# Kernel tuning notes

Hardware: AMD Instinct MI355X
Metric: run time of the kernel (lower is better)

Reference implementation:

```python
import jax, jax.numpy as jnp
import numpy as np

ROPE_THETA = 10000.0

def rope(x):
    # RoPE over the FULL model_dim (applied pre head-split, as in the source),
    # interleaved even/odd pairs. x: [B, S, D]
    B, S, D = x.shape
    half = D // 2
    inv_freq = 1.0 / (ROPE_THETA ** (jnp.arange(half, dtype=jnp.float32) * 2.0 / D))
    ang = jnp.arange(S, dtype=jnp.float32)[:, None] * inv_freq[None, :]  # [S, half]
    cos, sin = jnp.cos(ang), jnp.sin(ang)
    x1, x2 = x[..., 0::2], x[..., 1::2]
    r1 = x1 * cos - x2 * sin
    r2 = x1 * sin + x2 * cos
    return jnp.stack([r1, r2], axis=-1).reshape(B, S, D)


def setup_inputs() -> dict:
    key = jax.random.key(0)
    ks = jax.random.split(key, 9)
    B, S, D = 4, 2048, 768
    w = 0.02
    return {
        "X":  jax.random.normal(ks[0], (B, S, D), dtype=jnp.float32),
        "Wq": jax.random.normal(ks[1], (D, D), dtype=jnp.float32) * w,
        "bq": jnp.zeros((D,), dtype=jnp.float32),
        "Wk": jax.random.normal(ks[2], (D, D), dtype=jnp.float32) * w,
        "bk": jnp.zeros((D,), dtype=jnp.float32),
        "Wv": jax.random.normal(ks[3], (D, D), dtype=jnp.float32) * w,
        "bv": jnp.zeros((D,), dtype=jnp.float32),
        "Wo": jax.random.normal(ks[4], (D, D), dtype=jnp.float32) * w,
        "bo": jnp.zeros((D,), dtype=jnp.float32),
    }


def reference(X, Wq, bq, Wk, bk, Wv, bv, Wo, bo):
    NUM_HEADS = 12
    B, S, D = X.shape
    hd = D // NUM_HEADS

    q = rope(X @ Wq + bq)   # RoPE applied pre-split on full model_dim
    k = rope(X @ Wk + bk)
    v = X @ Wv + bv

    # Contiguous per-head slices == reshape to [B, S, H, hd]
    qh = q.reshape(B, S, NUM_HEADS, hd)
    kh = k.reshape(B, S, NUM_HEADS, hd)
    vh = v.reshape(B, S, NUM_HEADS, hd)

    scores = jnp.einsum('bqhd,bkhd->bhqk', qh, kh) / jnp.sqrt(jnp.float32(hd))
    causal = jnp.tril(jnp.ones((S, S), dtype=bool))
    scores = jnp.where(causal[None, None, :, :], scores, -jnp.inf)
    weights = jax.nn.softmax(scores, axis=-1)
    out = jnp.einsum('bhqk,bkhd->bqhd', weights, vh).reshape(B, S, D)
    return out @ Wo + bo
```

## Files before the change

### kernel.cpp

```cpp
#include <hip/hip_runtime.h>
#include <math.h>

#define D_MODEL 768
#define NUM_HEADS 12
#define HEAD_DIM 64
#define SEQ 2048
#define BATCH 4
#define MROWS (BATCH * SEQ)
#define HALF_D (D_MODEL / 2)

typedef __bf16    bf16x8 __attribute__((ext_vector_type(8)));
typedef _Float16  f16x4  __attribute__((ext_vector_type(4)));
typedef float     f32x4  __attribute__((ext_vector_type(4)));

__device__ __forceinline__ void gload_lds16(const void* gp, void* lp) {
    __builtin_amdgcn_global_load_lds(
        (const __attribute__((address_space(1))) unsigned int*)gp,
        (__attribute__((address_space(3))) unsigned int*)lp, 16, 0, 0);
}

__global__ __launch_bounds__(256)
void prep(const float* __restrict__ X, __bf16* __restrict__ Xb,
          const float* __restrict__ W0, const float* __restrict__ W1,
          const float* __restrict__ W2, const float* __restrict__ W3,
          __bf16* __restrict__ T0, __bf16* __restrict__ T1,
          __bf16* __restrict__ T2, __bf16* __restrict__ T3)
{
    __shared__ float t[64][65];
    const int n   = blockIdx.x;
    const int tid = threadIdx.x;

    if (n < 3072) {
        size_t i = ((size_t)n * 256 + tid) * 8;
        float4 u = *(const float4*)(X + i);
        float4 v = *(const float4*)(X + i + 4);
        bf16x8 o;
        o[0]=(__bf16)u.x; o[1]=(__bf16)u.y; o[2]=(__bf16)u.z; o[3]=(__bf16)u.w;
        o[4]=(__bf16)v.x; o[5]=(__bf16)v.y; o[6]=(__bf16)v.z; o[7]=(__bf16)v.w;
        *(bf16x8*)(Xb + i) = o;
    } else {
        int m = n - 3072;
        int z = m / 144;
        int rem = m - z * 144;
        int by = rem / 12, bx = rem % 12;
        const float* W = z == 0 ? W0 : z == 1 ? W1 : z == 2 ? W2 : W3;
        __bf16*      T = z == 0 ? T0 : z == 1 ? T1 : z == 2 ? T2 : T3;

        const int r0 = by * 64, c0 = bx * 64;
        const int lx = tid & 63, g = tid >> 6;

        #pragma unroll
        for (int rr = 0; rr < 16; ++rr) {
            int r = g * 16 + rr;
            t[r][lx] = W[(size_t)(r0 + r) * D_MODEL + c0 + lx];
        }
        __syncthreads();

        const int nn = tid >> 2;
        const int kb = (tid & 3) * 16;
        bf16x8 o1, o2;
        #pragma unroll
        for (int mm = 0; mm < 8; ++mm) o1[mm] = (__bf16)t[kb + mm][nn];
        #pragma unroll
        for (int mm = 0; mm < 8; ++mm) o2[mm] = (__bf16)t[kb + 8 + mm][nn];
        __bf16* dst = T + (size_t)(c0 + nn) * D_MODEL + r0 + kb;
        *(bf16x8*)dst       = o1;
        *(bf16x8*)(dst + 8) = o2;
    }
}

__global__ __launch_bounds__(512, 6)
void qkv_gemm(const __bf16* __restrict__ Xb,
              const __bf16* __restrict__ Wqt, const __bf16* __restrict__ Wkt,
              const __bf16* __restrict__ Wvt,
              const float* __restrict__ bq, const float* __restrict__ bk,
              const float* __restrict__ bv,
              __bf16* __restrict__ Qb, __bf16* __restrict__ Kb,
              _Float16* __restrict__ Vtb)
{
    __shared__ bf16x8 Asf[3][8][64];
    __shared__ bf16x8 Bsf[3][8][64];

    const int tid  = threadIdx.x;
    const int wv   = tid >> 6;
    const int ln   = tid & 63;
    const int t15  = ln & 15;
    const int quad = ln >> 4;
    const int wr = wv >> 2, wc = wv & 3;

    const int lin = blockIdx.x;
    const int c   = lin >> 6;
    const int r   = lin & 63;
    const int which = c / 6;
    const int col0  = (c % 6) * 128;
    const int row0  = r * 128;

    const __bf16* Wt  = which == 0 ? Wqt : which == 1 ? Wkt : Wvt;
    const float* bias = which == 0 ? bq  : which == 1 ? bk  : bv;

    f32x4 acc[4][2];
    #pragma unroll
    for (int i = 0; i < 4; ++i)
        #pragma unroll
        for (int j = 0; j < 2; ++j) acc[i][j] = (f32x4){0.f,0.f,0.f,0.f};

    const __bf16* seg[2];
    bf16x8*       dstp[2];
    #pragma unroll
    for (int u = 0; u < 2; ++u) {
        const int id   = wv * 2 + u;
        const int isB  = id >> 3;
        const int slot = id & 7;
        const __bf16* base = isB
            ? Wt + (size_t)(col0 + 16 * slot + t15) * D_MODEL
            : Xb + (size_t)(row0 + 16 * slot + t15) * D_MODEL;
        seg[u]  = base + 8 * quad;
        dstp[u] = isB ? &Bsf[0][slot][0] : &Asf[0][slot][0];
    }

    auto stage = [&](int buf, int k0) {
        #pragma unroll
        for (int u = 0; u < 2; ++u)
            gload_lds16(seg[u] + k0, dstp[u] + buf * 512);
    };

    stage(0, 0);
    stage(1, 32);

    const int NT = D_MODEL / 32;
    int cur = 0, nx = 2;
    for (int t = 0; t < NT; ++t) {
        if (t < NT - 1) { asm volatile("s_waitcnt vmcnt(2)" ::: "memory"); }
        else            { asm volatile("s_waitcnt vmcnt(0)" ::: "memory"); }
        __builtin_amdgcn_s_barrier();
        if (t + 2 < NT) stage(nx, 32 * (t + 2));

        bf16x8 af[4], bfr[2];
        #pragma unroll
        for (int i = 0; i < 4; ++i) af[i]  = Asf[cur][4 * wr + i][ln];
        #pragma unroll
        for (int j = 0; j < 2; ++j) bfr[j] = Bsf[cur][2 * wc + j][ln];
        #pragma unroll
        for (int i = 0; i < 4; ++i)
            #pragma unroll
            for (int j = 0; j < 2; ++j)
                acc[i][j] = __builtin_amdgcn_mfma_f32_16x16x32_bf16(af[i], bfr[j], acc[i][j], 0, 0, 0);

        cur = (cur == 2) ? 0 : cur + 1;
        nx  = (nx  == 2) ? 0 : nx  + 1;
    }

    if (which < 2) {
        const float oscale = (which == 0) ? 0.125f : 1.0f;
        __bf16* dstq = which ? Kb : Qb;
        #pragma unroll
        for (int i = 0; i < 4; ++i) {
            const int rowb = row0 + 64 * wr + 16 * i + 4 * quad;
            const int s0   = rowb & (SEQ - 1);
            #pragma unroll
            for (int j = 0; j < 2; ++j) {
                const int col = col0 + 32 * wc + 16 * j + t15;
                const float bval = bias[col];
                const int ne = col & ~1;
                const float fr = __expf((float)ne * (-9.210340371976184f / 768.0f));
                const float cf = __cosf(fr), sf = __sinf(fr);
                const float sgn = (col & 1) ? 1.0f : -1.0f;
                float ang = (float)s0 * fr;
                float ca = __cosf(ang), sa = __sinf(ang);
                #pragma unroll
                for (int rr = 0; rr < 4; ++rr) {
                    const int rw = rowb + rr;
                    float val  = acc[i][j][rr] + bval;
                    float part = __shfl_xor(val, 1, 64);
                    dstq[(size_t)rw * D_MODEL + col] = (__bf16)((val * ca + part * sgn * sa) * oscale);
                    float cn = ca * cf - sa * sf;
                    sa = sa * cf + ca * sf;
                    ca = cn;
                }
            }
        }
    } else {
        #pragma unroll
        for (int i = 0; i < 4; ++i) {
            const int rowb = row0 + 64 * wr + 16 * i + 4 * quad;
            #pragma unroll
            for (int j = 0; j < 2; ++j) {
                const int col = col0 + 32 * wc + 16 * j + t15;
                const float bval = bias[col];
                const int h = col >> 6, d = col & 63;
                const int bidx = rowb >> 11, s = rowb & (SEQ - 1);
                f16x4 pk;
                #pragma unroll
                for (int rr = 0; rr < 4; ++rr) pk[rr] = (_Float16)(acc[i][j][rr] + bval);
                *(f16x4*)(Vtb + ((size_t)(bidx * NUM_HEADS + h) * 64 + d) * SEQ + s) = pk;
            }
        }
    }
}

__global__ __launch_bounds__(256)
void out_gemm(const __bf16* __restrict__ Ab, const __bf16* __restrict__ Wt,
              const float* __restrict__ bias, float* __restrict__ Cout)
{
    __shared__ bf16x8 Asf[3][4][64];
    __shared__ bf16x8 Bsf[3][8][64];

    const int tid  = threadIdx.x;
    const int wv   = tid >> 6;
    const int ln   = tid & 63;
    const int t15  = ln & 15;
    const int quad = ln >> 4;
    const int wr = wv >> 1, wc = wv & 1;

    const int lin  = blockIdx.x;
    const int col0 = (lin >> 7) * 128;
    const int row0 = (lin & 127) * 64;

    f32x4 acc[2][4];
    #pragma unroll
    for (int i = 0; i < 2; ++i)
        #pragma unroll
        for (int j = 0; j < 4; ++j) acc[i][j] = (f32x4){0.f,0.f,0.f,0.f};

    auto stage = [&](int buf, int k0) {
        #pragma unroll
        for (int u = 0; u < 3; ++u) {
            const int id = wv * 3 + u;
            if (id < 4) {
                const __bf16* src = Ab + (size_t)(row0 + 16 * id + t15) * D_MODEL
                                       + k0 + 8 * quad;
                gload_lds16(src, &Asf[buf][id][0]);
            } else {
                const int w = id - 4;
                const __bf16* src = Wt + (size_t)(col0 + 16 * w + t15) * D_MODEL
                                       + k0 + 8 * quad;
                gload_lds16(src, &Bsf[buf][w][0]);
            }
        }
    };

    stage(0, 0);
    stage(1, 32);
    stage(2, 64);

    const int NT = D_MODEL / 32;
    int cur = 0;
    for (int t = 0; t < NT; ++t) {
        if (t + 2 < NT)      { asm volatile("s_waitcnt vmcnt(6)" ::: "memory"); }
        else if (t + 1 < NT) { asm volatile("s_waitcnt vmcnt(3)" ::: "memory"); }
        else                 { asm volatile("s_waitcnt vmcnt(0)" ::: "memory"); }
        __builtin_amdgcn_s_barrier();

        bf16x8 af[2], bfr[4];
        #pragma unroll
        for (int i = 0; i < 2; ++i) af[i]  = Asf[cur][2 * wr + i][ln];
        #pragma unroll
        for (int j = 0; j < 4; ++j) bfr[j] = Bsf[cur][4 * wc + j][ln];
        #pragma unroll
        for (int i = 0; i < 2; ++i)
            #pragma unroll
            for (int j = 0; j < 4; ++j)
                acc[i][j] = __builtin_amdgcn_mfma_f32_16x16x32_bf16(af[i], bfr[j], acc[i][j], 0, 0, 0);

        asm volatile("s_waitcnt lgkmcnt(0)" ::: "memory");
        __builtin_amdgcn_s_barrier();
        if (t + 3 < NT) stage(cur, 32 * (t + 3));
        cur = (cur == 2) ? 0 : cur + 1;
    }

    #pragma unroll
    for (int i = 0; i < 2; ++i) {
        const int rowb = row0 + 32 * wr + 16 * i + 4 * quad;
        #pragma unroll
        for (int j = 0; j < 4; ++j) {
            const int col = col0 + 64 * wc + 16 * j + t15;
            const float bval = bias[col];
            #pragma unroll
            for (int rr = 0; rr < 4; ++rr)
                Cout[(size_t)(rowb + rr) * D_MODEL + col] = acc[i][j][rr] + bval;
        }
    }
}

__device__ __forceinline__ void attn_tile(
    const bf16x8 (*Kbuf)[64], const _Float16* Vbuf ,
    bf16x8 aq0, bf16x8 aq1,
    f32x4* o, float& lacc,
    int ln, int t15, int quad, int j0, int qglob, bool domask)
{
    f32x4 s[4];
    #pragma unroll
    for (int c = 0; c < 4; ++c) {
        s[c] = (f32x4){0.f, 0.f, 0.f, 0.f};
        s[c] = __builtin_amdgcn_mfma_f32_16x16x32_bf16(Kbuf[c][ln],     aq0, s[c], 0, 0, 0);
        s[c] = __builtin_amdgcn_mfma_f32_16x16x32_bf16(Kbuf[4 + c][ln], aq1, s[c], 0, 0, 0);
    }

    f16x4 pf[4];
    #pragma unroll
    for (int c = 0; c < 4; ++c)
        #pragma unroll
        for (int r = 0; r < 4; ++r) {
            float e = __expf(s[c][r]);
            if (domask && (j0 + 16 * c + 4 * quad + r > qglob)) e = 0.f;
            lacc += e;
            pf[c][r] = (_Float16)e;
        }

    #pragma unroll
    for (int c = 0; c < 4; ++c) {
        const int lv = 16 * (2 * (c & 1) + (quad >> 1)) + t15;
        const int jb = 4 * (quad & 1);
        #pragma unroll
        for (int cd = 0; cd < 4; ++cd) {
            f16x4 vf = *(const f16x4*)&Vbuf[(size_t)(4 * (c >> 1) + cd) * 512 + lv * 8 + jb];
            o[cd] = __builtin_amdgcn_mfma_f32_16x16x16f16(pf[c], vf, o[cd], 0, 0, 0);
        }
    }
}

__global__ __launch_bounds__(512)
void attn_flash(const __bf16* __restrict__ Q, const __bf16* __restrict__ K,
                const _Float16* __restrict__ Vt, __bf16* __restrict__ O)
{
    __shared__ bf16x8   Kf[2][8][64];
    __shared__ _Float16 Vh[2][8][512];

    const int tid  = threadIdx.x;
    const int wv   = tid >> 6;
    const int ln   = tid & 63;
    const int t15  = ln & 15;
    const int quad = ln >> 4;

    const int n  = blockIdx.x;
    const int qt = 15 - (n / 48);
    const int bh = n % 48;
    const int b  = bh / NUM_HEADS;
    const int h  = bh % NUM_HEADS;
    const int q0 = qt * 128;
    const int nt = (q0 >> 6) + 2;

    bf16x8 aq0, aq1;
    {
        const __bf16* qs = Q + (size_t)(b * SEQ + q0 + 16 * wv + t15) * D_MODEL + h * 64 + 8 * quad;
        aq0 = *(const bf16x8*)qs;
        aq1 = *(const bf16x8*)(qs + 32);
    }

    const __bf16*   kp = K  + ((size_t)b * SEQ + 16 * (wv & 3) + t15) * D_MODEL
                            + h * 64 + 32 * (wv >> 2) + 8 * quad;
    const _Float16* vp = Vt + ((size_t)bh * 64 + 16 * (wv & 3) + t15) * SEQ
                            + 32 * (wv >> 2) + 8 * quad;

    f32x4 o[4];
    #pragma unroll
    for (int c = 0; c < 4; ++c) o[c] = (f32x4){0.f,0.f,0.f,0.f};
    float lacc = 0.f;
    const int qglob = q0 + 16 * wv + t15;
    const int wmax  = q0 + 16 * wv + 15;

    gload_lds16(kp, &Kf[0][wv][0]);
    gload_lds16(vp, &Vh[0][wv][0]);

    int cur = 0;
    for (int it = 0; it < nt; ++it) {
        __syncthreads();
        if (it + 1 < nt) {
            const int jn = (it + 1) * 64;
            gload_lds16(kp + (size_t)jn * D_MODEL, &Kf[cur ^ 1][wv][0]);
            gload_lds16(vp + jn,                   &Vh[cur ^ 1][wv][0]);
        }
        const int j0 = it * 64;
        if (j0 <= wmax) {
            const bool domask = (j0 + 63) > (q0 + 16 * wv);
            attn_tile(Kf[cur], &Vh[cur][0][0], aq0, aq1, o, lacc,
                      ln, t15, quad, j0, qglob, domask);
        }
        cur ^= 1;
    }

    lacc += __shfl_xor(lacc, 16, 64);
    lacc += __shfl_xor(lacc, 32, 64);

    float inv[4];
    #pragma unroll
    for (int r = 0; r < 4; ++r)
        inv[r] = 1.0f / __shfl(lacc, 4 * quad + r, 64);

    #pragma unroll
    for (int c = 0; c < 4; ++c)
        #pragma unroll
        for (int r = 0; r < 4; ++r) {
            int row = q0 + 16 * wv + 4 * quad + r;
            O[(size_t)(b * SEQ + row) * D_MODEL + h * 64 + 16 * c + t15] = (__bf16)(o[c][r] * inv[r]);
        }
}

extern "C" void kernel_launch(void* const* d_in, const int* in_sizes, int n_in,
                              void* d_out, int out_size, void* d_ws, size_t ws_size,
                              hipStream_t stream) {
    const float* X  = (const float*)d_in[0];
    const float* Wq = (const float*)d_in[1];
    const float* bq = (const float*)d_in[2];
    const float* Wk = (const float*)d_in[3];
    const float* bk = (const float*)d_in[4];
    const float* Wv = (const float*)d_in[5];
    const float* bv = (const float*)d_in[6];
    const float* Wo = (const float*)d_in[7];
    const float* bo = (const float*)d_in[8];
    float* out = (float*)d_out;

    const size_t BSD = (size_t)MROWS * D_MODEL;
    const size_t WSZ = (size_t)D_MODEL * D_MODEL;

    __bf16*   Xb  = (__bf16*)d_ws;
    __bf16*   Qb  = Xb  + BSD;
    __bf16*   Kb  = Qb  + BSD;
    _Float16* Vtb = (_Float16*)(Kb + BSD);
    __bf16*   Ob  = (__bf16*)(Vtb + BSD);
    __bf16*   Wqt = Ob  + BSD;
    __bf16*   Wkt = Wqt + WSZ;
    __bf16*   Wvt = Wkt + WSZ;
    __bf16*   Wot = Wvt + WSZ;

    prep<<<3648, 256, 0, stream>>>(X, Xb, Wq, Wk, Wv, Wo, Wqt, Wkt, Wvt, Wot);

    qkv_gemm<<<1152, 512, 0, stream>>>(Xb, Wqt, Wkt, Wvt, bq, bk, bv, Qb, Kb, Vtb);

    attn_flash<<<768, 512, 0, stream>>>(Qb, Kb, Vtb, Ob);

    out_gemm<<<768, 256, 0, stream>>>(Ob, Wot, bo, out);
}
```

Measured before the change: 236.3 us.

## Fuse QKV weights into one GEMM with 512x144 tiles and 256 blocks

Treats Wq, Wk and Wv as one contiguous 2304-column transposed weight, assumed to be laid out back to back in the workspace. The QKV projection now uses 512x144 output tiles, one tile per CU across 256 blocks, instead of 1152 blocks of 128x128. Each wave computes 64x144 with 36 accumulators, so reuse of the A operand rises and the per-column which-matrix dispatch moves into the epilogue. This adds register pressure (launch bounds lowered to 2), uneven load counts across waves, and a single wave of blocks with no tail balancing.

```diff
diff --git a/kernel.cpp b/kernel.cpp
--- a/kernel.cpp
+++ b/kernel.cpp
@@ -69,59 +69,61 @@
     }
 }
 
-__global__ __launch_bounds__(512, 6)
+__global__ __launch_bounds__(512, 2)
 void qkv_gemm(const __bf16* __restrict__ Xb,
-              const __bf16* __restrict__ Wqt, const __bf16* __restrict__ Wkt,
-              const __bf16* __restrict__ Wvt,
+              const __bf16* __restrict__ Wall,
               const float* __restrict__ bq, const float* __restrict__ bk,
               const float* __restrict__ bv,
               __bf16* __restrict__ Qb, __bf16* __restrict__ Kb,
               _Float16* __restrict__ Vtb)
 {
-    __shared__ bf16x8 Asf[3][8][64];
-    __shared__ bf16x8 Bsf[3][8][64];
+    __shared__ bf16x8 Asf[3][32][64];
+    __shared__ bf16x8 Bsf[3][9][64];
 
     const int tid  = threadIdx.x;
     const int wv   = tid >> 6;
     const int ln   = tid & 63;
     const int t15  = ln & 15;
     const int quad = ln >> 4;
-    const int wr = wv >> 2, wc = wv & 3;
-
-    const int lin = blockIdx.x;
-    const int c   = lin >> 6;
-    const int r   = lin & 63;
-    const int which = c / 6;
-    const int col0  = (c % 6) * 128;
-    const int row0  = r * 128;
-
-    const __bf16* Wt  = which == 0 ? Wqt : which == 1 ? Wkt : Wvt;
-    const float* bias = which == 0 ? bq  : which == 1 ? bk  : bv;
-
-    f32x4 acc[4][2];
+
+    const int lin  = blockIdx.x;
+    const int ct   = lin >> 4;
+    const int rt   = lin & 15;
+    const int col0 = ct * 144;
+    const int row0 = rt * 512;
+
+    f32x4 acc[4][9];
     #pragma unroll
     for (int i = 0; i < 4; ++i)
         #pragma unroll
-        for (int j = 0; j < 2; ++j) acc[i][j] = (f32x4){0.f,0.f,0.f,0.f};
-
-    const __bf16* seg[2];
-    bf16x8*       dstp[2];
-    #pragma unroll
-    for (int u = 0; u < 2; ++u) {
-        const int id   = wv * 2 + u;
-        const int isB  = id >> 3;
-        const int slot = id & 7;
-        const __bf16* base = isB
-            ? Wt + (size_t)(col0 + 16 * slot + t15) * D_MODEL
-            : Xb + (size_t)(row0 + 16 * slot + t15) * D_MODEL;
-        seg[u]  = base + 8 * quad;
-        dstp[u] = isB ? &Bsf[0][slot][0] : &Asf[0][slot][0];
+        for (int j = 0; j < 9; ++j) acc[i][j] = (f32x4){0.f,0.f,0.f,0.f};
+
+    const int NSEG = (wv == 0) ? 6 : 5;
+    const __bf16* seg[6];
+    bf16x8*       dstp[6];
+    int           bstr[6];
+    #pragma unroll
+    for (int u = 0; u < 4; ++u) {
+        const int slot = 4 * wv + u;
+        seg[u]  = Xb + (size_t)(row0 + 16 * slot + t15) * D_MODEL + 8 * quad;
+        dstp[u] = &Asf[0][slot][0];
+        bstr[u] = 32 * 64;
+    }
+    {
+        seg[4]  = Wall + (size_t)(col0 + 16 * wv + t15) * D_MODEL + 8 * quad;
+        dstp[4] = &Bsf[0][wv][0];
+        bstr[4] = 9 * 64;
+        seg[5]  = Wall + (size_t)(col0 + 16 * 8 + t15) * D_MODEL + 8 * quad;
+        dstp[5] = &Bsf[0][8][0];
+        bstr[5] = 9 * 64;
     }
 
     auto stage = [&](int buf, int k0) {
         #pragma unroll
-        for (int u = 0; u < 2; ++u)
-            gload_lds16(seg[u] + k0, dstp[u] + buf * 512);
+        for (int u = 0; u < 5; ++u)
+            gload_lds16(seg[u] + k0, dstp[u] + buf * bstr[u]);
+        if (wv == 0)
+            gload_lds16(seg[5] + k0, dstp[5] + buf * bstr[5]);
     };
 
     stage(0, 0);
@@ -130,41 +132,45 @@
     const int NT = D_MODEL / 32;
     int cur = 0, nx = 2;
     for (int t = 0; t < NT; ++t) {
-        if (t < NT - 1) { asm volatile("s_waitcnt vmcnt(2)" ::: "memory"); }
-        else            { asm volatile("s_waitcnt vmcnt(0)" ::: "memory"); }
+        if (t < NT - 1) {
+            if (wv == 0) { asm volatile("s_waitcnt vmcnt(6)" ::: "memory"); }
+            else         { asm volatile("s_waitcnt vmcnt(5)" ::: "memory"); }
+        } else           { asm volatile("s_waitcnt vmcnt(0)" ::: "memory"); }
         __builtin_amdgcn_s_barrier();
         if (t + 2 < NT) stage(nx, 32 * (t + 2));
 
-        bf16x8 af[4], bfr[2];
-        #pragma unroll
-        for (int i = 0; i < 4; ++i) af[i]  = Asf[cur][4 * wr + i][ln];
-        #pragma unroll
-        for (int j = 0; j < 2; ++j) bfr[j] = Bsf[cur][2 * wc + j][ln];
-        #pragma unroll
-        for (int i = 0; i < 4; ++i)
+        bf16x8 af[4];
+        #pragma unroll
+        for (int i = 0; i < 4; ++i) af[i] = Asf[cur][4 * wv + i][ln];
+        #pragma unroll
+        for (int j = 0; j < 9; ++j) {
+            bf16x8 bfr = Bsf[cur][j][ln];
             #pragma unroll
-            for (int j = 0; j < 2; ++j)
-                acc[i][j] = __builtin_amdgcn_mfma_f32_16x16x32_bf16(af[i], bfr[j], acc[i][j], 0, 0, 0);
+            for (int i = 0; i < 4; ++i)
+                acc[i][j] = __builtin_amdgcn_mfma_f32_16x16x32_bf16(af[i], bfr, acc[i][j], 0, 0, 0);
+        }
 
         cur = (cur == 2) ? 0 : cur + 1;
         nx  = (nx  == 2) ? 0 : nx  + 1;
     }
 
-    if (which < 2) {
-        const float oscale = (which == 0) ? 0.125f : 1.0f;
-        __bf16* dstq = which ? Kb : Qb;
-        #pragma unroll
-        for (int i = 0; i < 4; ++i) {
-            const int rowb = row0 + 64 * wr + 16 * i + 4 * quad;
-            const int s0   = rowb & (SEQ - 1);
-            #pragma unroll
-            for (int j = 0; j < 2; ++j) {
-                const int col = col0 + 32 * wc + 16 * j + t15;
-                const float bval = bias[col];
-                const int ne = col & ~1;
+    #pragma unroll
+    for (int i = 0; i < 4; ++i) {
+        const int rowb = row0 + 64 * wv + 16 * i + 4 * quad;
+        const int s0   = rowb & (SEQ - 1);
+        #pragma unroll
+        for (int j = 0; j < 9; ++j) {
+            const int col   = col0 + 16 * j + t15;
+            const int which = col / 768;
+            if (which < 2) {
+                const int qk = col - which * 768;
+                const float bval = (which == 0 ? bq : bk)[qk];
+                const float oscale = (which == 0) ? 0.125f : 1.0f;
+                __bf16* dstq = which ? Kb : Qb;
+                const int ne = qk & ~1;
                 const float fr = __expf((float)ne * (-9.210340371976184f / 768.0f));
                 const float cf = __cosf(fr), sf = __sinf(fr);
-                const float sgn = (col & 1) ? 1.0f : -1.0f;
+                const float sgn = (qk & 1) ? 1.0f : -1.0f;
                 float ang = (float)s0 * fr;
                 float ca = __cosf(ang), sa = __sinf(ang);
                 #pragma unroll
@@ -172,22 +178,15 @@
                     const int rw = rowb + rr;
                     float val  = acc[i][j][rr] + bval;
                     float part = __shfl_xor(val, 1, 64);
-                    dstq[(size_t)rw * D_MODEL + col] = (__bf16)((val * ca + part * sgn * sa) * oscale);
+                    dstq[(size_t)rw * D_MODEL + qk] = (__bf16)((val * ca + part * sgn * sa) * oscale);
                     float cn = ca * cf - sa * sf;
                     sa = sa * cf + ca * sf;
                     ca = cn;
                 }
-            }
-        }
-    } else {
-        #pragma unroll
-        for (int i = 0; i < 4; ++i) {
-            const int rowb = row0 + 64 * wr + 16 * i + 4 * quad;
-            #pragma unroll
-            for (int j = 0; j < 2; ++j) {
-                const int col = col0 + 32 * wc + 16 * j + t15;
-                const float bval = bias[col];
-                const int h = col >> 6, d = col & 63;
+            } else {
+                const int vcol = col - 1536;
+                const float bval = bv[vcol];
+                const int h = vcol >> 6, d = vcol & 63;
                 const int bidx = rowb >> 11, s = rowb & (SEQ - 1);
                 f16x4 pk;
                 #pragma unroll
@@ -425,7 +424,7 @@
 
     prep<<<3648, 256, 0, stream>>>(X, Xb, Wq, Wk, Wv, Wo, Wqt, Wkt, Wvt, Wot);
 
-    qkv_gemm<<<1152, 512, 0, stream>>>(Xb, Wqt, Wkt, Wvt, bq, bk, bv, Qb, Kb, Vtb);
+    qkv_gemm<<<256, 512, 0, stream>>>(Xb, Wqt, bq, bk, bv, Qb, Kb, Vtb);
 
     attn_flash<<<768, 512, 0, stream>>>(Qb, Kb, Vtb, Ob);
 
```

Result: no change. 234.0 us (-1.0%).
